# Performance work log

Measured on AMD Instinct MI355X. Metric: run time of the kernel, lower is better.

The kernel has to match this reference:

```python
import jax, jax.numpy as jnp
import numpy as np
from jax import lax


def _run_layer(x, h0, W_ih, W_hh, b_ih, b_hh):
    """Elman RNN layer. x: (S, B, F), h0: (B, H). Returns (ys: (S,B,H), hT: (B,H))."""
    Wih_T = W_ih.T  # (F, H)
    Whh_T = W_hh.T  # (H, H)

    def step(h, x_t):
        h_new = jnp.tanh(x_t @ Wih_T + b_ih + h @ Whh_T + b_hh)
        return h_new, h_new

    hT, ys = lax.scan(step, h0, x)
    return ys, hT


def setup_inputs() -> dict:
    key = jax.random.key(0)
    ks = jax.random.split(key, 8)
    S, B, I, H = 1024, 64, 512, 512
    stdv = 1.0 / np.sqrt(H)
    u = lambda k, shape: jax.random.uniform(k, shape, jnp.float32, -stdv, stdv)
    return {
        "x": jax.random.normal(ks[0], (S, B, I), jnp.float32),
        "hx": jnp.zeros((2, B, H), jnp.float32),
        "W_ih0": u(ks[1], (H, I)),
        "W_hh0": u(ks[2], (H, H)) ,
        "b_ih0": u(ks[3], (H,)),
        "b_hh0": jnp.zeros((H,), jnp.float32),
        "W_ih1": u(ks[4], (H, H)),
        "W_hh1": u(ks[5], (H, H)),
        "b_ih1": u(ks[6], (H,)),
        "b_hh1": jnp.zeros((H,), jnp.float32),
    }


def reference(x, hx, W_ih0, W_hh0, b_ih0, b_hh0, W_ih1, W_hh1, b_ih1, b_hh1):
    # Layer 0
    y0, h0T = _run_layer(x, hx[0], W_ih0, W_hh0, b_ih0, b_hh0)
    # Layer 1 (dropout=0.0 so layer input is y0 unchanged)
    y1, h1T = _run_layer(y0, hx[1], W_ih1, W_hh1, b_ih1, b_hh1)
    h_n = jnp.stack([h0T, h1T], axis=0)  # (num_layers, B, H)
    return y1, h_n
```

## Files before the change

kernel.cpp:

```cpp
#include <hip/hip_runtime.h>
#include <math.h>

#define SEQ 1024
#define BATCH 64
#define HID 512
#define MROWS (SEQ * BATCH)

#define SLICES 8
#define JW 64
#define NGROUPS 32
#define PSTRIDE ((size_t)NGROUPS * SLICES * 2 * JW)

typedef unsigned long long u64;
typedef unsigned int u32;

__launch_bounds__(256)
__global__ void transposeW(const float* __restrict__ W, float* __restrict__ Wt) {
    __shared__ float tile[32][33];
    int bx = blockIdx.x % 16;
    int by = blockIdx.x / 16;
    int tx = threadIdx.x % 32;
    int ty = threadIdx.x / 32;
    #pragma unroll
    for (int i = 0; i < 32; i += 8)
        tile[ty + i][tx] = W[(size_t)(by * 32 + ty + i) * HID + bx * 32 + tx];
    __syncthreads();
    #pragma unroll
    for (int i = 0; i < 32; i += 8)
        Wt[(size_t)(bx * 32 + ty + i) * HID + by * 32 + tx] = tile[tx][ty + i];
}

#define BM 64
#define BN 64
#define BK 16
__launch_bounds__(256)
__global__ void gemm_bias(const float* __restrict__ A, const float* __restrict__ W,
                          const float* __restrict__ b1, const float* __restrict__ b2,
                          float* __restrict__ C) {
    __shared__ float As[BK][BM + 4];
    __shared__ float Ws[BK][BN + 4];

    const int bj = blockIdx.x % (HID / BN);
    const int bi = blockIdx.x / (HID / BN);
    const int tid = threadIdx.x;
    const int tx = tid % 16;
    const int ty = tid / 16;
    const int row0 = bi * BM;
    const int col0 = bj * BN;

    const int lr = tid / 4;
    const int lk = (tid % 4) * 4;

    float acc[4][4] = {};

    for (int k0 = 0; k0 < HID; k0 += BK) {
        float4 av = *(const float4*)(A + (size_t)(row0 + lr) * HID + k0 + lk);
        float4 wv = *(const float4*)(W + (size_t)(col0 + lr) * HID + k0 + lk);
        As[lk + 0][lr] = av.x; As[lk + 1][lr] = av.y;
        As[lk + 2][lr] = av.z; As[lk + 3][lr] = av.w;
        Ws[lk + 0][lr] = wv.x; Ws[lk + 1][lr] = wv.y;
        Ws[lk + 2][lr] = wv.z; Ws[lk + 3][lr] = wv.w;
        __syncthreads();
        #pragma unroll
        for (int k = 0; k < BK; ++k) {
            float4 a = *(const float4*)&As[k][ty * 4];
            float4 w = *(const float4*)&Ws[k][tx * 4];
            acc[0][0] += a.x * w.x; acc[0][1] += a.x * w.y; acc[0][2] += a.x * w.z; acc[0][3] += a.x * w.w;
            acc[1][0] += a.y * w.x; acc[1][1] += a.y * w.y; acc[1][2] += a.y * w.z; acc[1][3] += a.y * w.w;
            acc[2][0] += a.z * w.x; acc[2][1] += a.z * w.y; acc[2][2] += a.z * w.z; acc[2][3] += a.z * w.w;
            acc[3][0] += a.w * w.x; acc[3][1] += a.w * w.y; acc[3][2] += a.w * w.z; acc[3][3] += a.w * w.w;
        }
        __syncthreads();
    }

    #pragma unroll
    for (int c = 0; c < 4; ++c) {
        int col = col0 + tx * 4 + c;
        float bias = b1[col] + b2[col];
        #pragma unroll
        for (int r = 0; r < 4; ++r) {
            C[(size_t)(row0 + ty * 4 + r) * HID + col] = acc[r][c] + bias;
        }
    }
}

__launch_bounds__(1024, 4)
__global__ void rnn_rec5(float* __restrict__ U,
                         const float* __restrict__ Wt,
                         const float* __restrict__ h0,
                         float* __restrict__ hT,
                         u64* __restrict__ hb)
{
    __shared__ __align__(16) float scratch[16][64];
    __shared__ float2 red[16][JW];
    __shared__ float  own[2][JW];

    const int blk = blockIdx.x;
    const int s = blk >> 5;
    const int g = blk & 31;
    const int j0 = s * JW;
    const int b0 = g * 2;
    const int tid = threadIdx.x;
    const int jl = tid & 63;
    const int kq = tid >> 6;

    float wreg[32];
    #pragma unroll
    for (int kk = 0; kk < 32; ++kk)
        wreg[kk] = Wt[(size_t)(kq * 32 + kk) * HID + j0 + jl];

    const int gk = kq * 32 + (jl >> 1);
    const int gb = jl & 1;
    const bool ownwave = ((kq >> 1) == s);
    const size_t gslot = (((size_t)g * SLICES + (gk >> 6)) * 2 + gb) * JW + (gk & 63);

    scratch[kq][jl] = h0[(size_t)(b0 + gb) * HID + gk];

    const int rb = (tid >> 6) & 1;
    const int rj = tid & 63;
    float u_pref = 0.f;
    if (tid < 128)
        u_pref = U[((size_t)0 * BATCH + (b0 + rb)) * HID + j0 + rj];

    for (int t = 0; t < SEQ; ++t) {
        float a0 = 0.f, a1 = 0.f;
        const float4* h4p = (const float4*)scratch[kq];
        #pragma unroll
        for (int q = 0; q < 16; ++q) {
            float4 h4 = h4p[q];
            a0 = fmaf(wreg[2 * q],     h4.x, a0);
            a1 = fmaf(wreg[2 * q],     h4.y, a1);
            a0 = fmaf(wreg[2 * q + 1], h4.z, a0);
            a1 = fmaf(wreg[2 * q + 1], h4.w, a1);
        }
        red[kq][jl] = make_float2(a0, a1);
        __syncthreads();

        const int p = (t + 1) & 1;
        const u32 tag = (u32)(t + 1);

        if (tid < 128) {
            float sum = 0.f;
            const float* rp = (const float*)red;
            #pragma unroll
            for (int q = 0; q < 16; ++q)
                sum += rp[(q * 64 + rj) * 2 + rb];
            float pre = u_pref + sum;
            u64 pkt = ((u64)__float_as_uint(pre) << 32) | tag;
            __hip_atomic_store(hb + p * PSTRIDE
                                  + (((size_t)g * SLICES + s) * 2 + rb) * JW + rj,
                               pkt, __ATOMIC_RELAXED, __HIP_MEMORY_SCOPE_AGENT);
            float v = tanhf(pre);
            U[((size_t)t * BATCH + (b0 + rb)) * HID + j0 + rj] = v;
            own[rb][rj] = v;
            const int tn = (t + 1 < SEQ) ? (t + 1) : t;
            u_pref = U[((size_t)tn * BATCH + (b0 + rb)) * HID + j0 + rj];
        }
        __syncthreads();

        if (t + 1 < SEQ) {
            float v;
            if (ownwave) {
                v = own[gb][gk & 63];
            } else {
                const u64* slot = hb + p * PSTRIDE + gslot;
                u64 pkt;
                int it = 0;
                do {
                    pkt = __hip_atomic_load(slot, __ATOMIC_RELAXED,
                                            __HIP_MEMORY_SCOPE_AGENT);
                } while ((u32)pkt != tag && ++it < (1 << 14));
                v = tanhf(__uint_as_float((u32)(pkt >> 32)));
            }
            scratch[kq][jl] = v;
        }
    }

    if (s == 0) {
        const int k = tid >> 1, b = tid & 1;
        const u32 tag = (u32)SEQ;
        const int p = SEQ & 1;
        const u64* slot = hb + p * PSTRIDE
                             + (((size_t)g * SLICES + (k >> 6)) * 2 + b) * JW + (k & 63);
        u64 pkt;
        int it = 0;
        do {
            pkt = __hip_atomic_load(slot, __ATOMIC_RELAXED, __HIP_MEMORY_SCOPE_AGENT);
        } while ((u32)pkt != tag && ++it < (1 << 14));
        hT[(size_t)(b0 + b) * HID + k] = tanhf(__uint_as_float((u32)(pkt >> 32)));
    }
}

extern "C" void kernel_launch(void* const* d_in, const int* in_sizes, int n_in,
                              void* d_out, int out_size, void* d_ws, size_t ws_size,
                              hipStream_t stream) {
    (void)in_sizes; (void)n_in; (void)out_size; (void)ws_size;

    const float* x      = (const float*)d_in[0];
    const float* hx     = (const float*)d_in[1];
    const float* W_ih0  = (const float*)d_in[2];
    const float* W_hh0  = (const float*)d_in[3];
    const float* b_ih0  = (const float*)d_in[4];
    const float* b_hh0  = (const float*)d_in[5];
    const float* W_ih1  = (const float*)d_in[6];
    const float* W_hh1  = (const float*)d_in[7];
    const float* b_ih1  = (const float*)d_in[8];
    const float* b_hh1  = (const float*)d_in[9];

    float* out = (float*)d_out;
    float* y1   = out;
    float* hT0  = out + (size_t)SEQ * BATCH * HID;
    float* hT1  = hT0 + (size_t)BATCH * HID;

    const size_t HB_ELTS = 2 * PSTRIDE;

    float* Wt0 = (float*)d_ws;
    float* Wt1 = Wt0 + (size_t)HID * HID;
    u64* hb0 = (u64*)(Wt1 + (size_t)HID * HID);
    u64* hb1 = hb0 + HB_ELTS;
    float* U0 = (float*)(hb1 + HB_ELTS);

    hipMemsetAsync(hb0, 0, 2 * HB_ELTS * sizeof(u64), stream);

    transposeW<<<256, 256, 0, stream>>>(W_hh0, Wt0);
    transposeW<<<256, 256, 0, stream>>>(W_hh1, Wt1);

    gemm_bias<<<(MROWS / BM) * (HID / BN), 256, 0, stream>>>(x, W_ih0, b_ih0, b_hh0, U0);

    rnn_rec5<<<NGROUPS * SLICES, 1024, 0, stream>>>(U0, Wt0, hx, hT0, hb0);

    gemm_bias<<<(MROWS / BM) * (HID / BN), 256, 0, stream>>>(U0, W_ih1, b_ih1, b_hh1, y1);

    rnn_rec5<<<NGROUPS * SLICES, 1024, 0, stream>>>(y1, Wt1, hx + (size_t)BATCH * HID, hT1, hb1);
}
```

Measured before the change: 3.847 ms.

## Replace block barriers with LDS counter sync and double-buffered reduction

Removes both __syncthreads per timestep in the recurrent kernel. Waves now signal through a workgroup-scope atomic counter, and a double-buffered reduction array lets waves move ahead without waiting for the reducer. The own-slice shortcut is dropped, so every wave polls the global packet buffer. It also uses packed 2-wide FMA and halves the spin bound. The price is more global polling traffic and a fragile spin-wait that relies on a timeout; the scratch buffer may be overwritten while other waves are still reading it.

```diff
diff --git a/kernel.cpp b/kernel.cpp
--- a/kernel.cpp
+++ b/kernel.cpp
@@ -13,6 +13,7 @@
 
 typedef unsigned long long u64;
 typedef unsigned int u32;
+typedef float f32x2 __attribute__((ext_vector_type(2)));
 
 __launch_bounds__(256)
 __global__ void transposeW(const float* __restrict__ W, float* __restrict__ Wt) {
@@ -85,15 +86,15 @@
 }
 
 __launch_bounds__(1024, 4)
-__global__ void rnn_rec5(float* __restrict__ U,
+__global__ void rnn_rec6(float* __restrict__ U,
                          const float* __restrict__ Wt,
                          const float* __restrict__ h0,
                          float* __restrict__ hT,
                          u64* __restrict__ hb)
 {
     __shared__ __align__(16) float scratch[16][64];
-    __shared__ float2 red[16][JW];
-    __shared__ float  own[2][JW];
+    __shared__ __align__(16) f32x2 red[2][16][64];
+    __shared__ u32 cnt;
 
     const int blk = blockIdx.x;
     const int s = blk >> 5;
@@ -111,37 +112,49 @@
 
     const int gk = kq * 32 + (jl >> 1);
     const int gb = jl & 1;
-    const bool ownwave = ((kq >> 1) == s);
     const size_t gslot = (((size_t)g * SLICES + (gk >> 6)) * 2 + gb) * JW + (gk & 63);
 
     scratch[kq][jl] = h0[(size_t)(b0 + gb) * HID + gk];
+    if (tid == 0) cnt = 0;
 
     const int rb = (tid >> 6) & 1;
     const int rj = tid & 63;
     float u_pref = 0.f;
     if (tid < 128)
         u_pref = U[((size_t)0 * BATCH + (b0 + rb)) * HID + j0 + rj];
+    __syncthreads();
 
     for (int t = 0; t < SEQ; ++t) {
-        float a0 = 0.f, a1 = 0.f;
+        const int wp = t & 1;
+        const int p  = (t + 1) & 1;
+        const u32 tag = (u32)(t + 1);
+
+        f32x2 acc = {0.f, 0.f};
         const float4* h4p = (const float4*)scratch[kq];
         #pragma unroll
         for (int q = 0; q < 16; ++q) {
             float4 h4 = h4p[q];
-            a0 = fmaf(wreg[2 * q],     h4.x, a0);
-            a1 = fmaf(wreg[2 * q],     h4.y, a1);
-            a0 = fmaf(wreg[2 * q + 1], h4.z, a0);
-            a1 = fmaf(wreg[2 * q + 1], h4.w, a1);
-        }
-        red[kq][jl] = make_float2(a0, a1);
-        __syncthreads();
-
-        const int p = (t + 1) & 1;
-        const u32 tag = (u32)(t + 1);
+            f32x2 hA = {h4.x, h4.y};
+            f32x2 hB = {h4.z, h4.w};
+            f32x2 wA = {wreg[2 * q],     wreg[2 * q]};
+            f32x2 wB = {wreg[2 * q + 1], wreg[2 * q + 1]};
+            acc = __builtin_elementwise_fma(wA, hA, acc);
+            acc = __builtin_elementwise_fma(wB, hB, acc);
+        }
+        red[wp][kq][jl] = acc;
+        if (jl == 0)
+            __hip_atomic_fetch_add(&cnt, 1u, __ATOMIC_RELEASE,
+                                   __HIP_MEMORY_SCOPE_WORKGROUP);
 
         if (tid < 128) {
+            const u32 target = 16u * (u32)(t + 1);
+            int gu = 0;
+            while (__hip_atomic_load(&cnt, __ATOMIC_ACQUIRE,
+                                     __HIP_MEMORY_SCOPE_WORKGROUP) < target) {
+                if (++gu > (1 << 16)) break;
+            }
             float sum = 0.f;
-            const float* rp = (const float*)red;
+            const float* rp = (const float*)red[wp];
             #pragma unroll
             for (int q = 0; q < 16; ++q)
                 sum += rp[(q * 64 + rj) * 2 + rb];
@@ -152,27 +165,19 @@
                                pkt, __ATOMIC_RELAXED, __HIP_MEMORY_SCOPE_AGENT);
             float v = tanhf(pre);
             U[((size_t)t * BATCH + (b0 + rb)) * HID + j0 + rj] = v;
-            own[rb][rj] = v;
             const int tn = (t + 1 < SEQ) ? (t + 1) : t;
             u_pref = U[((size_t)tn * BATCH + (b0 + rb)) * HID + j0 + rj];
         }
-        __syncthreads();
 
         if (t + 1 < SEQ) {
-            float v;
-            if (ownwave) {
-                v = own[gb][gk & 63];
-            } else {
-                const u64* slot = hb + p * PSTRIDE + gslot;
-                u64 pkt;
-                int it = 0;
-                do {
-                    pkt = __hip_atomic_load(slot, __ATOMIC_RELAXED,
-                                            __HIP_MEMORY_SCOPE_AGENT);
-                } while ((u32)pkt != tag && ++it < (1 << 14));
-                v = tanhf(__uint_as_float((u32)(pkt >> 32)));
-            }
-            scratch[kq][jl] = v;
+            const u64* slot = hb + p * PSTRIDE + gslot;
+            u64 pkt;
+            int it = 0;
+            do {
+                pkt = __hip_atomic_load(slot, __ATOMIC_RELAXED,
+                                        __HIP_MEMORY_SCOPE_AGENT);
+            } while ((u32)pkt != tag && ++it < (1 << 13));
+            scratch[kq][jl] = tanhf(__uint_as_float((u32)(pkt >> 32)));
         }
     }
 
@@ -186,7 +191,7 @@
         int it = 0;
         do {
             pkt = __hip_atomic_load(slot, __ATOMIC_RELAXED, __HIP_MEMORY_SCOPE_AGENT);
-        } while ((u32)pkt != tag && ++it < (1 << 14));
+        } while ((u32)pkt != tag && ++it < (1 << 13));
         hT[(size_t)(b0 + b) * HID + k] = tanhf(__uint_as_float((u32)(pkt >> 32)));
     }
 }
@@ -227,9 +232,9 @@
 
     gemm_bias<<<(MROWS / BM) * (HID / BN), 256, 0, stream>>>(x, W_ih0, b_ih0, b_hh0, U0);
 
-    rnn_rec5<<<NGROUPS * SLICES, 1024, 0, stream>>>(U0, Wt0, hx, hT0, hb0);
+    rnn_rec6<<<NGROUPS * SLICES, 1024, 0, stream>>>(U0, Wt0, hx, hT0, hb0);
 
     gemm_bias<<<(MROWS / BM) * (HID / BN), 256, 0, stream>>>(U0, W_ih1, b_ih1, b_hh1, y1);
 
-    rnn_rec5<<<NGROUPS * SLICES, 1024, 0, stream>>>(y1, Wt1, hx + (size_t)BATCH * HID, hT1, hb1);
-}
+    rnn_rec6<<<NGROUPS * SLICES, 1024, 0, stream>>>(y1, Wt1, hx + (size_t)BATCH * HID, hT1, hb1);
+}
```

After: 4.707 ms. 22.3% more time.
